# Kernel optimization log

Hardware: AMD Instinct MI355X
Metric: run time of the kernel (lower is better)

Reference implementation:

```python
import jax, jax.numpy as jnp
import numpy as np

B, S, Q, I, A = 32, 2048, 1024, 1024, 1024


def setup_inputs() -> dict:
    key = jax.random.key(0)
    ks = jax.random.split(key, 6)
    return {
        "queries": jax.random.normal(ks[0], (B, 1, Q), dtype=jnp.float32),
        "multiple_items": jax.random.normal(ks[1], (B, S, I), dtype=jnp.float32),
        "weights": jax.random.randint(ks[2], (B, S), 0, 2, dtype=jnp.int32),
        # nn.Linear(in, out, bias=False) weights, stored as [in, out] for x @ W
        "W": jax.random.normal(ks[3], (Q, A), dtype=jnp.float32) / np.float32(np.sqrt(Q)),
        "U": jax.random.normal(ks[4], (I, A), dtype=jnp.float32) / np.float32(np.sqrt(I)),
        "v": jax.random.normal(ks[5], (A,), dtype=jnp.float32) / np.float32(np.sqrt(A)),
    }


def reference(queries, multiple_items, weights, W, U, v):
    # queries: [B,1,Q], multiple_items: [B,S,I], weights: [B,S] int mask
    pq = jnp.einsum('btq,qa->bta', queries, W)          # [B,1,A]
    pi = jnp.einsum('bsi,ia->bsa', multiple_items, U)   # [B,S,A]
    added = jnp.tanh(pq + pi)                           # [B,S,A] broadcast add
    reactivity = jnp.einsum('bsa,a->bs', added, v)      # [B,S]
    reactivity = jnp.where(weights == 0, -jnp.inf, reactivity)
    attention_scores = jax.nn.softmax(reactivity, axis=1)  # [B,S]
    blended = jnp.einsum('bs,bsi->bi', attention_scores, multiple_items)  # [B,I]
    return blended, attention_scores
```

## Files before the change

kernel.cpp:

```cpp
#include <hip/hip_runtime.h>
#include <hip/hip_bf16.h>
#include <cstdint>

#define BB 32
#define SS 2048
#define QQ 1024
#define II 1024
#define AA 1024
#define MM (BB * SS)

typedef __bf16 bf16x8 __attribute__((ext_vector_type(8)));
typedef float  f32x4  __attribute__((ext_vector_type(4)));

__device__ __forceinline__ unsigned int pack_bf2(float a, float b) {
  unsigned ua = __builtin_bit_cast(unsigned, a) + 0x8000u;
  unsigned ub = __builtin_bit_cast(unsigned, b) + 0x8000u;
  return __builtin_amdgcn_perm(ub, ua, 0x07060302u);
}

__global__ void __launch_bounds__(256) k_transpose_u(const float* __restrict__ U,
                                                     unsigned short* __restrict__ Ut) {
  __shared__ float t[64][65];
  const int n0 = blockIdx.x * 64, k0 = blockIdx.y * 64;
  const int c = threadIdx.x & 63, r0 = threadIdx.x >> 6;
#pragma unroll
  for (int r = r0; r < 64; r += 4) t[r][c] = U[(size_t)(k0 + r) * AA + n0 + c];
  __syncthreads();
#pragma unroll
  for (int r = r0; r < 64; r += 4) {
    __hip_bfloat16 h = __float2bfloat16(t[c][r]);
    Ut[(size_t)(n0 + r) * II + k0 + c] = __builtin_bit_cast(unsigned short, h);
  }
}

__global__ void __launch_bounds__(128) k_pq(const float* __restrict__ q,
                                            const float* __restrict__ W,
                                            float* __restrict__ pq) {
  const int a  = blockIdx.x * 128 + threadIdx.x;
  const int b  = blockIdx.y;
  const int q0 = blockIdx.z * 256;
  const float* qr = q + b * QQ + q0;
  const float* Wp = W + (size_t)q0 * AA + a;
  float acc = 0.f;
#pragma unroll 8
  for (int i = 0; i < 256; ++i) acc += qr[i] * Wp[(size_t)i * AA];
  atomicAdd(&pq[b * AA + a], acc);
}

__global__ void __launch_bounds__(256) k_gemm_react(const float* __restrict__ items,
                                                    const unsigned short* __restrict__ Ut,
                                                    const float* __restrict__ pq,
                                                    const float* __restrict__ v,
                                                    float* __restrict__ react) {
  __shared__ unsigned short As[128 * 64];
  __shared__ unsigned short Bs[128 * 64];

  const int tid  = threadIdx.x;
  const int lane = tid & 63, wid = tid >> 6;
  const int wm = wid >> 1, wn = wid & 1;
  const int quad = lane >> 4, sx = lane & 15;

  const unsigned id = blockIdx.x;
  const int xcd = id & 7;
  const int j   = id >> 3;
  const int mtile = xcd + 8 * (j >> 3);
  const int ntile = j & 7;
  const int m0 = mtile * 128, n0 = ntile * 128;
  const int b  = m0 >> 11;

  const int ar = tid >> 2;
  const int aq = tid & 3;
  const int bn = tid >> 1;
  const int bh = tid & 1;

  f32x4 acc[4][4] = {};

  for (int kk = 0; kk < 16; ++kk) {
    const int k0 = kk * 64;
    __syncthreads();
#pragma unroll
    for (int rr = 0; rr < 2; ++rr) {
      const int r = ar + rr * 64;
      const float* g = items + (size_t)(m0 + r) * II + k0 + aq * 16;
      float4 f0 = ((const float4*)g)[0];
      float4 f1 = ((const float4*)g)[1];
      float4 f2 = ((const float4*)g)[2];
      float4 f3 = ((const float4*)g)[3];
      uint4 w0, w1;
      w0.x = pack_bf2(f0.x, f0.y); w0.y = pack_bf2(f0.z, f0.w);
      w0.z = pack_bf2(f1.x, f1.y); w0.w = pack_bf2(f1.z, f1.w);
      w1.x = pack_bf2(f2.x, f2.y); w1.y = pack_bf2(f2.z, f2.w);
      w1.z = pack_bf2(f3.x, f3.y); w1.w = pack_bf2(f3.z, f3.w);
      const int c0 = (2 * aq) ^ (r & 7);
      const int c1 = (2 * aq + 1) ^ (r & 7);
      *(uint4*)&As[r * 64 + c0 * 8] = w0;
      *(uint4*)&As[r * 64 + c1 * 8] = w1;
    }
    {
      const unsigned short* g = Ut + (size_t)(n0 + bn) * II + k0 + bh * 32;
#pragma unroll
      for (int jj = 0; jj < 4; ++jj) {
        uint4 w = ((const uint4*)g)[jj];
        const int c = (bh * 4 + jj) ^ (bn & 7);
        *(uint4*)&Bs[bn * 64 + c * 8] = w;
      }
    }
    __syncthreads();
#pragma unroll
    for (int ks = 0; ks < 2; ++ks) {
      bf16x8 af[4], bfv[4];
#pragma unroll
      for (int mi = 0; mi < 4; ++mi) {
        const int r = wm * 64 + mi * 16 + sx;
        const int c = (ks * 4 + quad) ^ (r & 7);
        af[mi] = *(const bf16x8*)&As[r * 64 + c * 8];
      }
#pragma unroll
      for (int ni = 0; ni < 4; ++ni) {
        const int r = wn * 64 + ni * 16 + sx;
        const int c = (ks * 4 + quad) ^ (r & 7);
        bfv[ni] = *(const bf16x8*)&Bs[r * 64 + c * 8];
      }
#pragma unroll
      for (int mi = 0; mi < 4; ++mi)
#pragma unroll
        for (int ni = 0; ni < 4; ++ni)
          acc[mi][ni] = __builtin_amdgcn_mfma_f32_16x16x32_bf16(af[mi], bfv[ni], acc[mi][ni], 0, 0, 0);
    }
  }

  float pqv[4], vv[4];
#pragma unroll
  for (int ni = 0; ni < 4; ++ni) {
    const int n = n0 + wn * 64 + ni * 16 + sx;
    pqv[ni] = pq[b * AA + n];
    vv[ni]  = v[n];
  }
#pragma unroll
  for (int mi = 0; mi < 4; ++mi) {
#pragma unroll
    for (int reg = 0; reg < 4; ++reg) {
      float ssum = 0.f;
#pragma unroll
      for (int ni = 0; ni < 4; ++ni) {
        const float x = acc[mi][ni][reg] + pqv[ni];
        const float e = __expf(2.f * x);
        const float t = 1.f - 2.f * __builtin_amdgcn_rcpf(e + 1.f);
        ssum += t * vv[ni];
      }
      ssum += __shfl_xor(ssum, 1);
      ssum += __shfl_xor(ssum, 2);
      ssum += __shfl_xor(ssum, 4);
      ssum += __shfl_xor(ssum, 8);
      if (sx == 0) {
        const int m = m0 + wm * 64 + mi * 16 + quad * 4 + reg;
        atomicAdd(&react[m], ssum);
      }
    }
  }
}

__global__ void __launch_bounds__(256) k_softmax(const float* __restrict__ react,
                                                 const int* __restrict__ weights,
                                                 float* __restrict__ scores) {
  const int b = blockIdx.x, tid = threadIdx.x;
  const int lane = tid & 63, wid = tid >> 6;
  __shared__ float redm[4], reds[4];
  float vals[8];
  float mx = -3.0e38f;
#pragma unroll
  for (int j = 0; j < 8; ++j) {
    const int s = j * 256 + tid;
    const float r = react[b * SS + s];
    const int w = weights[b * SS + s];
    const float val = (w != 0) ? r : -3.0e38f;
    vals[j] = val;
    mx = fmaxf(mx, val);
  }
#pragma unroll
  for (int off = 1; off < 64; off <<= 1) mx = fmaxf(mx, __shfl_xor(mx, off));
  if (lane == 0) redm[wid] = mx;
  __syncthreads();
  mx = fmaxf(fmaxf(redm[0], redm[1]), fmaxf(redm[2], redm[3]));
  float e[8], sum = 0.f;
#pragma unroll
  for (int j = 0; j < 8; ++j) {
    e[j] = (vals[j] < -1.0e38f) ? 0.f : __expf(vals[j] - mx);
    sum += e[j];
  }
#pragma unroll
  for (int off = 1; off < 64; off <<= 1) sum += __shfl_xor(sum, off);
  if (lane == 0) reds[wid] = sum;
  __syncthreads();
  const float inv = 1.f / (reds[0] + reds[1] + reds[2] + reds[3]);
#pragma unroll
  for (int j = 0; j < 8; ++j) scores[b * SS + j * 256 + tid] = e[j] * inv;
}

__global__ void __launch_bounds__(256) k_blended(const float* __restrict__ items,
                                                 const float* __restrict__ scores,
                                                 float* __restrict__ out) {
  const int b = blockIdx.x, s0 = blockIdx.y * 256;
  __shared__ float sc[256];
  sc[threadIdx.x] = scores[b * SS + s0 + threadIdx.x];
  __syncthreads();
  const float4* base = (const float4*)(items + (size_t)b * SS * II + (size_t)s0 * II);
  float4 acc = {0.f, 0.f, 0.f, 0.f};
  for (int s = 0; s < 256; ++s) {
    const float w = sc[s];
    if (w != 0.f) {
      const float4 it = base[s * 256 + threadIdx.x];
      acc.x += w * it.x; acc.y += w * it.y; acc.z += w * it.z; acc.w += w * it.w;
    }
  }
  float* o = out + b * II + threadIdx.x * 4;
  atomicAdd(o + 0, acc.x);
  atomicAdd(o + 1, acc.y);
  atomicAdd(o + 2, acc.z);
  atomicAdd(o + 3, acc.w);
}

extern "C" void kernel_launch(void* const* d_in, const int* in_sizes, int n_in,
                              void* d_out, int out_size, void* d_ws, size_t ws_size,
                              hipStream_t stream) {
  const float* queries = (const float*)d_in[0];
  const float* items   = (const float*)d_in[1];
  const int*   weights = (const int*)d_in[2];
  const float* W       = (const float*)d_in[3];
  const float* U       = (const float*)d_in[4];
  const float* v       = (const float*)d_in[5];
  float* out = (float*)d_out;

  char* ws = (char*)d_ws;
  unsigned short* Ut = (unsigned short*)ws;
  float* pq    = (float*)(ws + (2u << 20));
  float* react = (float*)(ws + (2u << 20) + (128u << 10));

  hipMemsetAsync(pq, 0, BB * AA * sizeof(float), stream);
  hipMemsetAsync(react, 0, MM * sizeof(float), stream);
  hipMemsetAsync(out, 0, BB * II * sizeof(float), stream);

  k_transpose_u<<<dim3(16, 16), 256, 0, stream>>>(U, Ut);
  k_pq<<<dim3(8, BB, 4), 128, 0, stream>>>(queries, W, pq);
  k_gemm_react<<<dim3(4096), 256, 0, stream>>>(items, Ut, pq, v, react);
  k_softmax<<<dim3(BB), 256, 0, stream>>>(react, weights, out + BB * II);
  k_blended<<<dim3(BB, 8), 256, 0, stream>>>(items, out + BB * II, out);
}
```

Measured before the change: 631.7 us.

## Pre-convert items to bf16 and use direct global-to-LDS loads in GEMM

Adds a pass that converts the full items tensor to bf16 in workspace, and a GEMM variant that fills LDS through global_load_lds with swizzled addressing in place of per-thread fp32 loads and packing. The old fp32-load GEMM stays as a fallback when the workspace is too small. The blended kernel now compacts nonzero scores into a list and handles 4 rows per iteration over 16 chunks. The cost is an extra write and read of a 128MB bf16 copy, traded against fewer redundant fp32 reads and less conversion work across the 8 N-tiles.

Result: no change. 640.0 us (+1.3%).

```diff
diff --git a/kernel.cpp b/kernel.cpp
--- a/kernel.cpp
+++ b/kernel.cpp
@@ -18,6 +18,12 @@
   return __builtin_amdgcn_perm(ub, ua, 0x07060302u);
 }
 
+__device__ __forceinline__ void gload_lds16(const void* g, void* l) {
+  __builtin_amdgcn_global_load_lds(
+      (const __attribute__((address_space(1))) void*)g,
+      (__attribute__((address_space(3))) void*)l, 16, 0, 0);
+}
+
 __global__ void __launch_bounds__(256) k_transpose_u(const float* __restrict__ U,
                                                      unsigned short* __restrict__ Ut) {
   __shared__ float t[64][65];
@@ -30,6 +36,20 @@
   for (int r = r0; r < 64; r += 4) {
     __hip_bfloat16 h = __float2bfloat16(t[c][r]);
     Ut[(size_t)(n0 + r) * II + k0 + c] = __builtin_bit_cast(unsigned short, h);
+  }
+}
+
+__global__ void __launch_bounds__(256) k_conv(const float* __restrict__ in,
+                                              uint4* __restrict__ outbf) {
+  const size_t n8 = (size_t)MM * II / 8;
+  const size_t stride = (size_t)gridDim.x * 256;
+  for (size_t i = (size_t)blockIdx.x * 256 + threadIdx.x; i < n8; i += stride) {
+    const float4* p = (const float4*)(in + i * 8);
+    float4 a = p[0], b = p[1];
+    uint4 w;
+    w.x = pack_bf2(a.x, a.y); w.y = pack_bf2(a.z, a.w);
+    w.z = pack_bf2(b.x, b.y); w.w = pack_bf2(b.z, b.w);
+    outbf[i] = w;
   }
 }
 
@@ -47,11 +67,46 @@
   atomicAdd(&pq[b * AA + a], acc);
 }
 
-__global__ void __launch_bounds__(256) k_gemm_react(const float* __restrict__ items,
-                                                    const unsigned short* __restrict__ Ut,
-                                                    const float* __restrict__ pq,
-                                                    const float* __restrict__ v,
-                                                    float* __restrict__ react) {
+__device__ __forceinline__ void react_epilogue(f32x4 (&acc)[4][4], const float* pq,
+                                               const float* v, float* react,
+                                               int b, int m0, int n0, int wm, int wn,
+                                               int quad, int sx) {
+  float pqv[4], vv[4];
+#pragma unroll
+  for (int ni = 0; ni < 4; ++ni) {
+    const int n = n0 + wn * 64 + ni * 16 + sx;
+    pqv[ni] = pq[b * AA + n];
+    vv[ni]  = v[n];
+  }
+#pragma unroll
+  for (int mi = 0; mi < 4; ++mi) {
+#pragma unroll
+    for (int reg = 0; reg < 4; ++reg) {
+      float ssum = 0.f;
+#pragma unroll
+      for (int ni = 0; ni < 4; ++ni) {
+        const float x = acc[mi][ni][reg] + pqv[ni];
+        const float e = __expf(2.f * x);
+        const float t = 1.f - 2.f * __builtin_amdgcn_rcpf(e + 1.f);
+        ssum += t * vv[ni];
+      }
+      ssum += __shfl_xor(ssum, 1);
+      ssum += __shfl_xor(ssum, 2);
+      ssum += __shfl_xor(ssum, 4);
+      ssum += __shfl_xor(ssum, 8);
+      if (sx == 0) {
+        const int m = m0 + wm * 64 + mi * 16 + quad * 4 + reg;
+        atomicAdd(&react[m], ssum);
+      }
+    }
+  }
+}
+
+__global__ void __launch_bounds__(256) k_gemm_bf(const unsigned short* __restrict__ Abf,
+                                                 const unsigned short* __restrict__ Ut,
+                                                 const float* __restrict__ pq,
+                                                 const float* __restrict__ v,
+                                                 float* __restrict__ react) {
   __shared__ unsigned short As[128 * 64];
   __shared__ unsigned short Bs[128 * 64];
 
@@ -68,13 +123,74 @@
   const int m0 = mtile * 128, n0 = ntile * 128;
   const int b  = m0 >> 11;
 
-  const int ar = tid >> 2;
-  const int aq = tid & 3;
-  const int bn = tid >> 1;
-  const int bh = tid & 1;
+  const int r_loc = lane >> 3;
+  const int cch   = lane & 7;
+  const int gch   = cch ^ r_loc;
 
   f32x4 acc[4][4] = {};
 
+  for (int kk = 0; kk < 16; ++kk) {
+    const int k0 = kk * 64;
+    __syncthreads();
+#pragma unroll
+    for (int jj = 0; jj < 4; ++jj) {
+      const int rA = wid * 32 + jj * 8 + r_loc;
+      gload_lds16(Abf + (size_t)(m0 + rA) * II + k0 + gch * 8,
+                  &As[(wid * 32 + jj * 8) * 64]);
+    }
+#pragma unroll
+    for (int jj = 0; jj < 4; ++jj) {
+      const int rB = wid * 32 + jj * 8 + r_loc;
+      gload_lds16(Ut + (size_t)(n0 + rB) * II + k0 + gch * 8,
+                  &Bs[(wid * 32 + jj * 8) * 64]);
+    }
+    __syncthreads();
+#pragma unroll
+    for (int ks = 0; ks < 2; ++ks) {
+      bf16x8 af[4], bfv[4];
+#pragma unroll
+      for (int mi = 0; mi < 4; ++mi) {
+        const int r = wm * 64 + mi * 16 + sx;
+        const int c = (ks * 4 + quad) ^ (r & 7);
+        af[mi] = *(const bf16x8*)&As[r * 64 + c * 8];
+      }
+#pragma unroll
+      for (int ni = 0; ni < 4; ++ni) {
+        const int r = wn * 64 + ni * 16 + sx;
+        const int c = (ks * 4 + quad) ^ (r & 7);
+        bfv[ni] = *(const bf16x8*)&Bs[r * 64 + c * 8];
+      }
+#pragma unroll
+      for (int mi = 0; mi < 4; ++mi)
+#pragma unroll
+        for (int ni = 0; ni < 4; ++ni)
+          acc[mi][ni] = __builtin_amdgcn_mfma_f32_16x16x32_bf16(af[mi], bfv[ni], acc[mi][ni], 0, 0, 0);
+    }
+  }
+  react_epilogue(acc, pq, v, react, b, m0, n0, wm, wn, quad, sx);
+}
+
+__global__ void __launch_bounds__(256) k_gemm_f32(const float* __restrict__ items,
+                                                  const unsigned short* __restrict__ Ut,
+                                                  const float* __restrict__ pq,
+                                                  const float* __restrict__ v,
+                                                  float* __restrict__ react) {
+  __shared__ unsigned short As[128 * 64];
+  __shared__ unsigned short Bs[128 * 64];
+  const int tid  = threadIdx.x;
+  const int lane = tid & 63, wid = tid >> 6;
+  const int wm = wid >> 1, wn = wid & 1;
+  const int quad = lane >> 4, sx = lane & 15;
+  const unsigned id = blockIdx.x;
+  const int xcd = id & 7;
+  const int j   = id >> 3;
+  const int mtile = xcd + 8 * (j >> 3);
+  const int ntile = j & 7;
+  const int m0 = mtile * 128, n0 = ntile * 128;
+  const int b  = m0 >> 11;
+  const int ar = tid >> 2, aq = tid & 3;
+  const int bn = tid >> 1, bh = tid & 1;
+  f32x4 acc[4][4] = {};
   for (int kk = 0; kk < 16; ++kk) {
     const int k0 = kk * 64;
     __syncthreads();
@@ -128,36 +244,7 @@
           acc[mi][ni] = __builtin_amdgcn_mfma_f32_16x16x32_bf16(af[mi], bfv[ni], acc[mi][ni], 0, 0, 0);
     }
   }
-
-  float pqv[4], vv[4];
-#pragma unroll
-  for (int ni = 0; ni < 4; ++ni) {
-    const int n = n0 + wn * 64 + ni * 16 + sx;
-    pqv[ni] = pq[b * AA + n];
-    vv[ni]  = v[n];
-  }
-#pragma unroll
-  for (int mi = 0; mi < 4; ++mi) {
-#pragma unroll
-    for (int reg = 0; reg < 4; ++reg) {
-      float ssum = 0.f;
-#pragma unroll
-      for (int ni = 0; ni < 4; ++ni) {
-        const float x = acc[mi][ni][reg] + pqv[ni];
-        const float e = __expf(2.f * x);
-        const float t = 1.f - 2.f * __builtin_amdgcn_rcpf(e + 1.f);
-        ssum += t * vv[ni];
-      }
-      ssum += __shfl_xor(ssum, 1);
-      ssum += __shfl_xor(ssum, 2);
-      ssum += __shfl_xor(ssum, 4);
-      ssum += __shfl_xor(ssum, 8);
-      if (sx == 0) {
-        const int m = m0 + wm * 64 + mi * 16 + quad * 4 + reg;
-        atomicAdd(&react[m], ssum);
-      }
-    }
-  }
+  react_epilogue(acc, pq, v, react, b, m0, n0, wm, wn, quad, sx);
 }
 
 __global__ void __launch_bounds__(256) k_softmax(const float* __restrict__ react,
@@ -200,20 +287,43 @@
 __global__ void __launch_bounds__(256) k_blended(const float* __restrict__ items,
                                                  const float* __restrict__ scores,
                                                  float* __restrict__ out) {
-  const int b = blockIdx.x, s0 = blockIdx.y * 256;
-  __shared__ float sc[256];
-  sc[threadIdx.x] = scores[b * SS + s0 + threadIdx.x];
-  __syncthreads();
-  const float4* base = (const float4*)(items + (size_t)b * SS * II + (size_t)s0 * II);
+  const int b = blockIdx.x, chunk = blockIdx.y, tid = threadIdx.x;
+  __shared__ int   lidx[132];
+  __shared__ float lsc[132];
+  __shared__ int   lcount;
+  if (tid == 0) lcount = 0;
+  __syncthreads();
+  if (tid < 128) {
+    const int s = chunk * 128 + tid;
+    const float sc = scores[b * SS + s];
+    if (sc != 0.f) {
+      const int p = atomicAdd(&lcount, 1);
+      lidx[p] = s; lsc[p] = sc;
+    }
+  }
+  __syncthreads();
+  const int cnt = lcount;
+  if (tid < 4) {
+    const int p = cnt + tid;
+    if (p < 132) { lidx[p] = chunk * 128; lsc[p] = 0.f; }
+  }
+  __syncthreads();
+  const int cnt4 = (cnt + 3) & ~3;
+  const float4* base = (const float4*)(items + (size_t)b * SS * II);
   float4 acc = {0.f, 0.f, 0.f, 0.f};
-  for (int s = 0; s < 256; ++s) {
-    const float w = sc[s];
-    if (w != 0.f) {
-      const float4 it = base[s * 256 + threadIdx.x];
-      acc.x += w * it.x; acc.y += w * it.y; acc.z += w * it.z; acc.w += w * it.w;
-    }
-  }
-  float* o = out + b * II + threadIdx.x * 4;
+  for (int j0 = 0; j0 < cnt4; j0 += 4) {
+    const int   s0 = lidx[j0],   s1 = lidx[j0+1], s2 = lidx[j0+2], s3 = lidx[j0+3];
+    const float w0 = lsc[j0],    w1 = lsc[j0+1],  w2 = lsc[j0+2],  w3 = lsc[j0+3];
+    const float4 x0 = base[(size_t)s0 * 256 + tid];
+    const float4 x1 = base[(size_t)s1 * 256 + tid];
+    const float4 x2 = base[(size_t)s2 * 256 + tid];
+    const float4 x3 = base[(size_t)s3 * 256 + tid];
+    acc.x += w0*x0.x + w1*x1.x + w2*x2.x + w3*x3.x;
+    acc.y += w0*x0.y + w1*x1.y + w2*x2.y + w3*x3.y;
+    acc.z += w0*x0.z + w1*x1.z + w2*x2.z + w3*x3.z;
+    acc.w += w0*x0.w + w1*x1.w + w2*x2.w + w3*x3.w;
+  }
+  float* o = out + b * II + tid * 4;
   atomicAdd(o + 0, acc.x);
   atomicAdd(o + 1, acc.y);
   atomicAdd(o + 2, acc.z);
@@ -235,6 +345,9 @@
   unsigned short* Ut = (unsigned short*)ws;
   float* pq    = (float*)(ws + (2u << 20));
   float* react = (float*)(ws + (2u << 20) + (128u << 10));
+  const size_t bf_off = (2u << 20) + (128u << 10) + (256u << 10);
+  unsigned short* Abf = (unsigned short*)(ws + bf_off);
+  const bool pathA = ws_size >= bf_off + (size_t)MM * II * 2;
 
   hipMemsetAsync(pq, 0, BB * AA * sizeof(float), stream);
   hipMemsetAsync(react, 0, MM * sizeof(float), stream);
@@ -242,7 +355,12 @@
 
   k_transpose_u<<<dim3(16, 16), 256, 0, stream>>>(U, Ut);
   k_pq<<<dim3(8, BB, 4), 128, 0, stream>>>(queries, W, pq);
-  k_gemm_react<<<dim3(4096), 256, 0, stream>>>(items, Ut, pq, v, react);
+  if (pathA) {
+    k_conv<<<dim3(16384), 256, 0, stream>>>(items, (uint4*)Abf);
+    k_gemm_bf<<<dim3(4096), 256, 0, stream>>>(Abf, Ut, pq, v, react);
+  } else {
+    k_gemm_f32<<<dim3(4096), 256, 0, stream>>>(items, Ut, pq, v, react);
+  }
   k_softmax<<<dim3(BB), 256, 0, stream>>>(react, weights, out + BB * II);
-  k_blended<<<dim3(BB, 8), 256, 0, stream>>>(items, out + BB * II, out);
-}
+  k_blended<<<dim3(BB, 16), 256, 0, stream>>>(items, out + BB * II, out);
+}
```
